# Kernel optimization log

Measured on AMD Instinct MI355X. Metric: run time of the kernel, lower is better.

The kernel has to match this reference:

```python
import jax, jax.numpy as jnp
import numpy as np

B = 256
IN_F = 1024
OUT_F = 1024
SUB_F = 128
Q_F = 1024
N_SUB = 64
N_ACT = 8


def setup_inputs() -> dict:
    key = jax.random.key(0)
    ks = jax.random.split(key, 6)
    x = jax.random.normal(ks[0], (B, IN_F), dtype=jnp.float32)
    q = jax.random.normal(ks[1], (B, Q_F), dtype=jnp.float32)
    # k_layer: nn.Linear(q_features, num_subnets) -> weight [S, Qf], bias [S]
    bound = 1.0 / np.sqrt(Q_F)
    Wk = jax.random.uniform(ks[2], (N_SUB, Q_F), jnp.float32, -bound, bound)
    bk = jax.random.uniform(ks[3], (N_SUB,), jnp.float32, -bound, bound)
    # V_0: [S, sub, in], V_1: [S, out, sub] initialized with randn (as in source)
    V0 = jax.random.normal(ks[4], (N_SUB, SUB_F, IN_F), dtype=jnp.float32)
    V1 = jax.random.normal(ks[5], (N_SUB, OUT_F, SUB_F), dtype=jnp.float32)
    return {"x": x, "q": q, "Wk": Wk, "bk": bk, "V0": V0, "V1": V1}


def _topk_mask(att, k):
    # 0 at top-k positions, -inf elsewhere (per row)
    _, idx = jax.lax.top_k(att, k)  # [B, k]
    mask = jnp.full_like(att, -jnp.inf)
    rows = jnp.arange(att.shape[0])[:, None]
    return mask.at[rows, idx].set(0.0)


def reference(x, q, Wk, bk, V0, V1):
    attention = q @ Wk.T + bk                         # [B, S]
    mask = _topk_mask(attention, N_ACT)               # [B, S]
    sparse_attention = jax.nn.softmax(attention + mask, axis=1)  # [B, S]
    V = jnp.einsum('sor,sri->soi', V1, V0)            # [S, out, in] (bmm)
    weights = jnp.einsum('bs,soi->boi', sparse_attention, V)     # [B, out, in]
    return jnp.einsum('boi,bi->bo', weights, x)       # [B, out]
```

## Files before the change

kernel.cpp:

```cpp
#include <hip/hip_runtime.h>
#include <math.h>

#define NB   256
#define NIN  1024
#define NOUT 1024
#define NSF  128
#define NQ   1024
#define NS   64
#define NACT 8
#define NSLOT 64
#define NIC  4

#define WS_COUNTS 0
#define WS_LISTBK 1024
#define WS_LISTW  17408
#define WS_Y      33792
#define WS_H      8422400

typedef __attribute__((ext_vector_type(8))) short bfrag;
typedef __attribute__((ext_vector_type(4))) float f4_t;

__device__ inline void bsplit(float f, ushort& h, ushort& l) {
    unsigned u = __builtin_bit_cast(unsigned, f);
    h = (ushort)(u >> 16);
    float hf = __builtin_bit_cast(float, u & 0xffff0000u);
    float lo = f - hf;
    l = (ushort)(__builtin_bit_cast(unsigned, lo) >> 16);
}
__device__ inline unsigned bpack(ushort a, ushort b) {
    return (unsigned)a | ((unsigned)b << 16);
}

__global__ __launch_bounds__(256) void attn_topk(
    const float* __restrict__ q, const float* __restrict__ Wk,
    const float* __restrict__ bk, int* __restrict__ counts,
    int* __restrict__ list_bk, float* __restrict__ list_w)
{
    int b = blockIdx.x;
    int t = threadIdx.x;

    __shared__ float qs[NQ];
    __shared__ float att[NS];

    ((float4*)qs)[t] = ((const float4*)(q + (size_t)b * NQ))[t];
    __syncthreads();

    int sid = t >> 2;
    int il  = t & 3;
    const float* wrow = Wk + (size_t)sid * NQ + (il << 2);
    const float* qrow = qs + (il << 2);
    float acc = 0.f;
    #pragma unroll 8
    for (int i = 0; i < NQ; i += 16) {
        float4 w4 = *(const float4*)(wrow + i);
        float4 q4 = *(const float4*)(qrow + i);
        acc += w4.x * q4.x + w4.y * q4.y + w4.z * q4.z + w4.w * q4.w;
    }
    acc += __shfl_xor(acc, 1);
    acc += __shfl_xor(acc, 2);
    if (il == 0) att[sid] = acc + bk[sid];
    __syncthreads();

    if (t < 64) {
        float v = att[t];
        float top_v[NACT]; int top_i[NACT];
        #pragma unroll
        for (int k = 0; k < NACT; ++k) {
            float mv = v; int mi = t;
            #pragma unroll
            for (int off = 1; off < 64; off <<= 1) {
                float ov = __shfl_xor(mv, off);
                int   oi = __shfl_xor(mi, off);
                if (ov > mv || (ov == mv && oi < mi)) { mv = ov; mi = oi; }
            }
            top_v[k] = mv; top_i[k] = mi;
            if (t == mi) v = -INFINITY;
        }
        if (t == 0) {
            float m = top_v[0], den = 0.f, e[NACT];
            #pragma unroll
            for (int k = 0; k < NACT; ++k) { e[k] = expf(top_v[k] - m); den += e[k]; }
            float inv = 1.f / den;
            #pragma unroll
            for (int k = 0; k < NACT; ++k) {
                int s = top_i[k];
                int slot = atomicAdd(&counts[s], 1);
                if (slot < NSLOT) {
                    list_bk[s * NSLOT + slot] = b * NACT + k;
                    list_w[s * NSLOT + slot]  = e[k] * inv;
                }
            }
        }
    }
}

__global__ __launch_bounds__(256) void subnet_h(
    const float* __restrict__ x, const float* __restrict__ V0,
    const int* __restrict__ counts, const int* __restrict__ list_bk,
    float* __restrict__ Hpart)
{
    int s  = blockIdx.x;
    int ic = blockIdx.y;
    int jt = blockIdx.z;
    int nb = counts[s]; if (nb > NSLOT) nb = NSLOT;
    if (jt * 32 >= nb) return;
    int t = threadIdx.x;

    __shared__ __align__(16) ushort vhi[128 * 64], vlo[128 * 64];
    __shared__ __align__(16) ushort xhi[32 * 64],  xlo[32 * 64];
    __shared__ int bidx[32];

    if (t < 32) {
        int idx = jt * 32 + t;
        bidx[t] = (idx < nb) ? (list_bk[s * NSLOT + idx] >> 3) : 0;
    }
    __syncthreads();

    int i0 = ic * 256;
    const float* V0s = V0 + (size_t)s * NSF * NIN;

    int lane = t & 63, w = t >> 6;
    int wo = w >> 1, wj = w & 1;
    int l15 = lane & 15, l4 = lane >> 4;
    int kk = l4 << 3;

    int tr = t >> 4;
    int k4 = (t & 15) << 2;

    int bj0 = bidx[tr], bj1 = bidx[16 + tr];

    float4 va[8], vb[2];
    f4_t acc[4] = {};

    #pragma unroll
    for (int rep = 0; rep < 8; ++rep)
        va[rep] = *(const float4*)(V0s + (size_t)(rep * 16 + tr) * NIN + i0 + k4);
    vb[0] = *(const float4*)(x + (size_t)bj0 * NIN + i0 + k4);
    vb[1] = *(const float4*)(x + (size_t)bj1 * NIN + i0 + k4);

    for (int kc = 0; kc < 256; kc += 64) {
        #pragma unroll
        for (int rep = 0; rep < 8; ++rep) {
            int row = rep * 16 + tr;
            float4 v = va[rep];
            ushort h0,l0,h1,l1,h2,l2,h3,l3;
            bsplit(v.x,h0,l0); bsplit(v.y,h1,l1); bsplit(v.z,h2,l2); bsplit(v.w,h3,l3);
            int hw = ((row << 6) + k4) ^ ((row & 7) << 3);
            *(uint2*)&vhi[hw] = make_uint2(bpack(h0,h1), bpack(h2,h3));
            *(uint2*)&vlo[hw] = make_uint2(bpack(l0,l1), bpack(l2,l3));
        }
        #pragma unroll
        for (int rep = 0; rep < 2; ++rep) {
            int j = rep * 16 + tr;
            float4 v = vb[rep];
            ushort h0,l0,h1,l1,h2,l2,h3,l3;
            bsplit(v.x,h0,l0); bsplit(v.y,h1,l1); bsplit(v.z,h2,l2); bsplit(v.w,h3,l3);
            int hw = ((j << 6) + k4) ^ ((j & 7) << 3);
            *(uint2*)&xhi[hw] = make_uint2(bpack(h0,h1), bpack(h2,h3));
            *(uint2*)&xlo[hw] = make_uint2(bpack(l0,l1), bpack(l2,l3));
        }
        __syncthreads();

        if (kc < 192) {
            int kn = i0 + kc + 64;
            #pragma unroll
            for (int rep = 0; rep < 8; ++rep)
                va[rep] = *(const float4*)(V0s + (size_t)(rep * 16 + tr) * NIN + kn + k4);
            vb[0] = *(const float4*)(x + (size_t)bj0 * NIN + kn + k4);
            vb[1] = *(const float4*)(x + (size_t)bj1 * NIN + kn + k4);
        }

        #pragma unroll
        for (int ks = 0; ks < 64; ks += 32) {
            int jrow = wj * 16 + l15;
            int bhw = ((jrow << 6) + ks + kk) ^ ((jrow & 7) << 3);
            bfrag bh = *(const bfrag*)&xhi[bhw];
            bfrag bl = *(const bfrag*)&xlo[bhw];
            #pragma unroll
            for (int f = 0; f < 4; ++f) {
                int row = wo * 64 + f * 16 + l15;
                int ahw = ((row << 6) + ks + kk) ^ ((row & 7) << 3);
                bfrag ah = *(const bfrag*)&vhi[ahw];
                bfrag al = *(const bfrag*)&vlo[ahw];
                acc[f] = __builtin_amdgcn_mfma_f32_16x16x32_bf16(ah, bh, acc[f], 0, 0, 0);
                acc[f] = __builtin_amdgcn_mfma_f32_16x16x32_bf16(ah, bl, acc[f], 0, 0, 0);
                acc[f] = __builtin_amdgcn_mfma_f32_16x16x32_bf16(al, bh, acc[f], 0, 0, 0);
            }
        }
        __syncthreads();
    }

    int jloc = wj * 16 + l15;
    float* Hp = Hpart + ((size_t)(ic * NS + s) * NSLOT + jt * 32 + jloc) * NSF;
    #pragma unroll
    for (int f = 0; f < 4; ++f) {
        *(float4*)(Hp + wo * 64 + f * 16 + (l4 << 2)) =
            make_float4(acc[f][0], acc[f][1], acc[f][2], acc[f][3]);
    }
}

__global__ __launch_bounds__(256) void subnet_out(
    const float* __restrict__ V1, const int* __restrict__ counts,
    const int* __restrict__ list_bk, const float* __restrict__ list_w,
    const float* __restrict__ Hpart, float* __restrict__ Ybuf)
{
    int s  = blockIdx.x;
    int ot = blockIdx.y;
    int jt = blockIdx.z;
    int nb = counts[s]; if (nb > NSLOT) nb = NSLOT;
    if (jt * 32 >= nb) return;
    int t = threadIdx.x;

    __shared__ __align__(16) ushort vhi[128 * 64], vlo[128 * 64];
    __shared__ __align__(16) ushort hhi[32 * 64],  hlo[32 * 64];
    __shared__ int   bkx[32];
    __shared__ float wjs[32];

    if (t < 32) {
        int idx = jt * 32 + t;
        bool v = idx < nb;
        bkx[t] = v ? list_bk[s * NSLOT + idx] : 0;
        wjs[t] = v ? list_w[s * NSLOT + idx] : 0.f;
    }
    __syncthreads();

    const float* V1s = V1 + (size_t)s * NOUT * NSF + (size_t)ot * 128 * NSF;
    const float* Hp  = Hpart + ((size_t)s * NSLOT + jt * 32) * NSF;
    const size_t HSTR = (size_t)NS * NSLOT * NSF;

    int lane = t & 63, w = t >> 6;
    int wo = w >> 1, wj = w & 1;
    int l15 = lane & 15, l4 = lane >> 4;
    int kk = l4 << 3;

    int tr = t >> 4;
    int k4 = (t & 15) << 2;

    float4 va[8], vb[8];
    f4_t acc[4] = {};

    #pragma unroll
    for (int rep = 0; rep < 8; ++rep)
        va[rep] = *(const float4*)(V1s + (size_t)(rep * 16 + tr) * NSF + k4);
    #pragma unroll
    for (int rep = 0; rep < 2; ++rep) {
        const float* hp = Hp + (size_t)(rep * 16 + tr) * NSF + k4;
        vb[rep * 4 + 0] = *(const float4*)(hp);
        vb[rep * 4 + 1] = *(const float4*)(hp + HSTR);
        vb[rep * 4 + 2] = *(const float4*)(hp + 2 * HSTR);
        vb[rep * 4 + 3] = *(const float4*)(hp + 3 * HSTR);
    }

    for (int kc = 0; kc < NSF; kc += 64) {
        #pragma unroll
        for (int rep = 0; rep < 8; ++rep) {
            int row = rep * 16 + tr;
            float4 v = va[rep];
            ushort h0,l0,h1,l1,h2,l2,h3,l3;
            bsplit(v.x,h0,l0); bsplit(v.y,h1,l1); bsplit(v.z,h2,l2); bsplit(v.w,h3,l3);
            int hw = ((row << 6) + k4) ^ ((row & 7) << 3);
            *(uint2*)&vhi[hw] = make_uint2(bpack(h0,h1), bpack(h2,h3));
            *(uint2*)&vlo[hw] = make_uint2(bpack(l0,l1), bpack(l2,l3));
        }
        #pragma unroll
        for (int rep = 0; rep < 2; ++rep) {
            int j = rep * 16 + tr;
            float4 u0 = vb[rep * 4 + 0], u1 = vb[rep * 4 + 1];
            float4 u2 = vb[rep * 4 + 2], u3 = vb[rep * 4 + 3];
            float4 v = make_float4(u0.x+u1.x+u2.x+u3.x, u0.y+u1.y+u2.y+u3.y,
                                   u0.z+u1.z+u2.z+u3.z, u0.w+u1.w+u2.w+u3.w);
            ushort h0,l0,h1,l1,h2,l2,h3,l3;
            bsplit(v.x,h0,l0); bsplit(v.y,h1,l1); bsplit(v.z,h2,l2); bsplit(v.w,h3,l3);
            int hw = ((j << 6) + k4) ^ ((j & 7) << 3);
            *(uint2*)&hhi[hw] = make_uint2(bpack(h0,h1), bpack(h2,h3));
            *(uint2*)&hlo[hw] = make_uint2(bpack(l0,l1), bpack(l2,l3));
        }
        __syncthreads();

        if (kc == 0) {
            #pragma unroll
            for (int rep = 0; rep < 8; ++rep)
                va[rep] = *(const float4*)(V1s + (size_t)(rep * 16 + tr) * NSF + 64 + k4);
            #pragma unroll
            for (int rep = 0; rep < 2; ++rep) {
                const float* hp = Hp + (size_t)(rep * 16 + tr) * NSF + 64 + k4;
                vb[rep * 4 + 0] = *(const float4*)(hp);
                vb[rep * 4 + 1] = *(const float4*)(hp + HSTR);
                vb[rep * 4 + 2] = *(const float4*)(hp + 2 * HSTR);
                vb[rep * 4 + 3] = *(const float4*)(hp + 3 * HSTR);
            }
        }

        #pragma unroll
        for (int ks = 0; ks < 64; ks += 32) {
            int jrow = wj * 16 + l15;
            int bhw = ((jrow << 6) + ks + kk) ^ ((jrow & 7) << 3);
            bfrag bh = *(const bfrag*)&hhi[bhw];
            bfrag bl = *(const bfrag*)&hlo[bhw];
            #pragma unroll
            for (int f = 0; f < 4; ++f) {
                int row = wo * 64 + f * 16 + l15;
                int ahw = ((row << 6) + ks + kk) ^ ((row & 7) << 3);
                bfrag ah = *(const bfrag*)&vhi[ahw];
                bfrag al = *(const bfrag*)&vlo[ahw];
                acc[f] = __builtin_amdgcn_mfma_f32_16x16x32_bf16(ah, bh, acc[f], 0, 0, 0);
                acc[f] = __builtin_amdgcn_mfma_f32_16x16x32_bf16(ah, bl, acc[f], 0, 0, 0);
                acc[f] = __builtin_amdgcn_mfma_f32_16x16x32_bf16(al, bh, acc[f], 0, 0, 0);
            }
        }
        __syncthreads();
    }

    int jloc = wj * 16 + l15;
    int slot = jt * 32 + jloc;
    if (slot < nb) {
        int   bki = bkx[jloc];
        float wgt = wjs[jloc];
        float* dst = Ybuf + (size_t)bki * NOUT + ot * 128 + wo * 64 + (l4 << 2);
        #pragma unroll
        for (int f = 0; f < 4; ++f) {
            *(float4*)(dst + f * 16) =
                make_float4(wgt*acc[f][0], wgt*acc[f][1], wgt*acc[f][2], wgt*acc[f][3]);
        }
    }
}

__global__ __launch_bounds__(256) void reduce_out(
    const float* __restrict__ Ybuf, float* __restrict__ out)
{
    int b = blockIdx.x, t = threadIdx.x;
    const float* yb = Ybuf + (size_t)b * NACT * NOUT + (t << 2);
    float4 a = *(const float4*)yb;
    #pragma unroll
    for (int k = 1; k < NACT; ++k) {
        float4 v = *(const float4*)(yb + (size_t)k * NOUT);
        a.x += v.x; a.y += v.y; a.z += v.z; a.w += v.w;
    }
    *(float4*)(out + (size_t)b * NOUT + (t << 2)) = a;
}

extern "C" void kernel_launch(void* const* d_in, const int* in_sizes, int n_in,
                              void* d_out, int out_size, void* d_ws, size_t ws_size,
                              hipStream_t stream)
{
    const float* x  = (const float*)d_in[0];
    const float* q  = (const float*)d_in[1];
    const float* Wk = (const float*)d_in[2];
    const float* bk = (const float*)d_in[3];
    const float* V0 = (const float*)d_in[4];
    const float* V1 = (const float*)d_in[5];
    float* out = (float*)d_out;

    char* ws = (char*)d_ws;
    int*   counts  = (int*)(ws + WS_COUNTS);
    int*   list_bk = (int*)(ws + WS_LISTBK);
    float* list_w  = (float*)(ws + WS_LISTW);
    float* Ybuf    = (float*)(ws + WS_Y);
    float* Hpart   = (float*)(ws + WS_H);

    hipMemsetAsync(counts, 0, 1024, stream);

    attn_topk<<<dim3(NB), 256, 0, stream>>>(q, Wk, bk, counts, list_bk, list_w);
    subnet_h<<<dim3(NS, NIC, 2), 256, 0, stream>>>(x, V0, counts, list_bk, Hpart);
    subnet_out<<<dim3(NS, 8, 2), 256, 0, stream>>>(V1, counts, list_bk, list_w, Hpart, Ybuf);
    reduce_out<<<dim3(NB), 256, 0, stream>>>(Ybuf, out);
}
```

Baseline: 145.1 us.

## Replace atomic per-subnet lists with per-block scan of top-k indices

The attention kernel now writes each row's top-k subnet indices and softmax weights densely, with no atomics, which removes the memset and atomic list-building. Each consumer block rebuilds its subnet's batch list itself with a wavefront prefix scan over all top-k indices, so list order becomes deterministic. subnet_h is also re-tiled into smaller 128-thread blocks that each cover half the sub-feature rows, doubling the grid for more parallelism. The cost is redundant scanning work in every block and extra reloading of x tiles across the row splits.

```diff
diff --git a/kernel.cpp b/kernel.cpp
--- a/kernel.cpp
+++ b/kernel.cpp
@@ -11,11 +11,10 @@
 #define NSLOT 64
 #define NIC  4
 
-#define WS_COUNTS 0
-#define WS_LISTBK 1024
-#define WS_LISTW  17408
-#define WS_Y      33792
-#define WS_H      8422400
+#define WS_TOPKS 0
+#define WS_TOPKW 2048
+#define WS_Y     10240
+#define WS_H     8398848
 
 typedef __attribute__((ext_vector_type(8))) short bfrag;
 typedef __attribute__((ext_vector_type(4))) float f4_t;
@@ -33,8 +32,8 @@
 
 __global__ __launch_bounds__(256) void attn_topk(
     const float* __restrict__ q, const float* __restrict__ Wk,
-    const float* __restrict__ bk, int* __restrict__ counts,
-    int* __restrict__ list_bk, float* __restrict__ list_w)
+    const float* __restrict__ bk, unsigned char* __restrict__ topk_s,
+    float* __restrict__ topk_w)
 {
     int b = blockIdx.x;
     int t = threadIdx.x;
@@ -81,67 +80,111 @@
             #pragma unroll
             for (int k = 0; k < NACT; ++k) { e[k] = expf(top_v[k] - m); den += e[k]; }
             float inv = 1.f / den;
-            #pragma unroll
-            for (int k = 0; k < NACT; ++k) {
-                int s = top_i[k];
-                int slot = atomicAdd(&counts[s], 1);
-                if (slot < NSLOT) {
-                    list_bk[s * NSLOT + slot] = b * NACT + k;
-                    list_w[s * NSLOT + slot]  = e[k] * inv;
-                }
-            }
-        }
-    }
-}
-
-__global__ __launch_bounds__(256) void subnet_h(
+            unsigned lo = (unsigned)top_i[0] | ((unsigned)top_i[1] << 8) |
+                          ((unsigned)top_i[2] << 16) | ((unsigned)top_i[3] << 24);
+            unsigned hi = (unsigned)top_i[4] | ((unsigned)top_i[5] << 8) |
+                          ((unsigned)top_i[6] << 16) | ((unsigned)top_i[7] << 24);
+            *(uint2*)(topk_s + (size_t)b * 8) = make_uint2(lo, hi);
+            *(float4*)(topk_w + (size_t)b * 8) =
+                make_float4(e[0]*inv, e[1]*inv, e[2]*inv, e[3]*inv);
+            *(float4*)(topk_w + (size_t)b * 8 + 4) =
+                make_float4(e[4]*inv, e[5]*inv, e[6]*inv, e[7]*inv);
+        }
+    }
+}
+
+__device__ inline void scan_subnet(const unsigned char* topk_s, int s, int t,
+                                   int* ent, int* nb_sh)
+{
+    if (t < 64) {
+        const uint2* ts = (const uint2*)topk_s;
+        uint2 rows[4];
+        #pragma unroll
+        for (int i = 0; i < 4; ++i) rows[i] = ts[t * 4 + i];
+        int cnt = 0;
+        #pragma unroll
+        for (int i = 0; i < 4; ++i) {
+            unsigned lo = rows[i].x, hi = rows[i].y;
+            #pragma unroll
+            for (int k = 0; k < 4; ++k) {
+                cnt += ((int)((lo >> (8*k)) & 0xff) == s);
+                cnt += ((int)((hi >> (8*k)) & 0xff) == s);
+            }
+        }
+        int p = cnt;
+        #pragma unroll
+        for (int off = 1; off < 64; off <<= 1) {
+            int v = __shfl_up(p, off);
+            if (t >= off) p += v;
+        }
+        int pos = p - cnt;
+        int tot = __shfl(p, 63);
+        int nb  = tot > NSLOT ? NSLOT : tot;
+        if (t == 0) *nb_sh = nb;
+        #pragma unroll
+        for (int i = 0; i < 4; ++i) {
+            unsigned lo = rows[i].x, hi = rows[i].y;
+            int b = t * 4 + i;
+            #pragma unroll
+            for (int k = 0; k < 8; ++k) {
+                int sv = (k < 4) ? (int)((lo >> (8*k)) & 0xff)
+                                 : (int)((hi >> (8*(k-4))) & 0xff);
+                if (sv == s) { if (pos < NSLOT) ent[pos] = b * 8 + k; ++pos; }
+            }
+        }
+        if (t >= nb) ent[t] = 0;
+    }
+}
+
+__global__ __launch_bounds__(128) void subnet_h(
     const float* __restrict__ x, const float* __restrict__ V0,
-    const int* __restrict__ counts, const int* __restrict__ list_bk,
-    float* __restrict__ Hpart)
+    const unsigned char* __restrict__ topk_s, float* __restrict__ Hpart)
 {
     int s  = blockIdx.x;
     int ic = blockIdx.y;
-    int jt = blockIdx.z;
-    int nb = counts[s]; if (nb > NSLOT) nb = NSLOT;
+    int rt = blockIdx.z >> 1;
+    int jt = blockIdx.z & 1;
+    int t = threadIdx.x;
+
+    __shared__ __align__(16) ushort vhi[64 * 64], vlo[64 * 64];
+    __shared__ __align__(16) ushort xhi[32 * 64], xlo[32 * 64];
+    __shared__ int ent[NSLOT];
+    __shared__ int nb_sh;
+
+    scan_subnet(topk_s, s, t, ent, &nb_sh);
+    __syncthreads();
+    int nb = nb_sh;
     if (jt * 32 >= nb) return;
-    int t = threadIdx.x;
-
-    __shared__ __align__(16) ushort vhi[128 * 64], vlo[128 * 64];
-    __shared__ __align__(16) ushort xhi[32 * 64],  xlo[32 * 64];
-    __shared__ int bidx[32];
-
-    if (t < 32) {
-        int idx = jt * 32 + t;
-        bidx[t] = (idx < nb) ? (list_bk[s * NSLOT + idx] >> 3) : 0;
-    }
-    __syncthreads();
 
     int i0 = ic * 256;
-    const float* V0s = V0 + (size_t)s * NSF * NIN;
-
-    int lane = t & 63, w = t >> 6;
-    int wo = w >> 1, wj = w & 1;
+    const float* V0s = V0 + ((size_t)s * NSF + rt * 64) * NIN;
+
+    int lane = t & 63;
+    int wj = t >> 6;
     int l15 = lane & 15, l4 = lane >> 4;
     int kk = l4 << 3;
 
     int tr = t >> 4;
     int k4 = (t & 15) << 2;
 
-    int bj0 = bidx[tr], bj1 = bidx[16 + tr];
-
-    float4 va[8], vb[2];
+    int bj[4];
+    #pragma unroll
+    for (int rep = 0; rep < 4; ++rep) bj[rep] = ent[jt * 32 + rep * 8 + tr] >> 3;
+
+    float4 va[8], vb[4];
     f4_t acc[4] = {};
 
     #pragma unroll
     for (int rep = 0; rep < 8; ++rep)
-        va[rep] = *(const float4*)(V0s + (size_t)(rep * 16 + tr) * NIN + i0 + k4);
-    vb[0] = *(const float4*)(x + (size_t)bj0 * NIN + i0 + k4);
-    vb[1] = *(const float4*)(x + (size_t)bj1 * NIN + i0 + k4);
+        va[rep] = *(const float4*)(V0s + (size_t)(rep * 8 + tr) * NIN + i0 + k4);
+    #pragma unroll
+    for (int rep = 0; rep < 4; ++rep)
+        vb[rep] = *(const float4*)(x + (size_t)bj[rep] * NIN + i0 + k4);
 
     for (int kc = 0; kc < 256; kc += 64) {
         #pragma unroll
         for (int rep = 0; rep < 8; ++rep) {
-            int row = rep * 16 + tr;
+            int row = rep * 8 + tr;
             float4 v = va[rep];
             ushort h0,l0,h1,l1,h2,l2,h3,l3;
             bsplit(v.x,h0,l0); bsplit(v.y,h1,l1); bsplit(v.z,h2,l2); bsplit(v.w,h3,l3);
@@ -150,8 +193,8 @@
             *(uint2*)&vlo[hw] = make_uint2(bpack(l0,l1), bpack(l2,l3));
         }
         #pragma unroll
-        for (int rep = 0; rep < 2; ++rep) {
-            int j = rep * 16 + tr;
+        for (int rep = 0; rep < 4; ++rep) {
+            int j = rep * 8 + tr;
             float4 v = vb[rep];
             ushort h0,l0,h1,l1,h2,l2,h3,l3;
             bsplit(v.x,h0,l0); bsplit(v.y,h1,l1); bsplit(v.z,h2,l2); bsplit(v.w,h3,l3);
@@ -165,9 +208,10 @@
             int kn = i0 + kc + 64;
             #pragma unroll
             for (int rep = 0; rep < 8; ++rep)
-                va[rep] = *(const float4*)(V0s + (size_t)(rep * 16 + tr) * NIN + kn + k4);
-            vb[0] = *(const float4*)(x + (size_t)bj0 * NIN + kn + k4);
-            vb[1] = *(const float4*)(x + (size_t)bj1 * NIN + kn + k4);
+                va[rep] = *(const float4*)(V0s + (size_t)(rep * 8 + tr) * NIN + kn + k4);
+            #pragma unroll
+            for (int rep = 0; rep < 4; ++rep)
+                vb[rep] = *(const float4*)(x + (size_t)bj[rep] * NIN + kn + k4);
         }
 
         #pragma unroll
@@ -178,7 +222,7 @@
             bfrag bl = *(const bfrag*)&xlo[bhw];
             #pragma unroll
             for (int f = 0; f < 4; ++f) {
-                int row = wo * 64 + f * 16 + l15;
+                int row = f * 16 + l15;
                 int ahw = ((row << 6) + ks + kk) ^ ((row & 7) << 3);
                 bfrag ah = *(const bfrag*)&vhi[ahw];
                 bfrag al = *(const bfrag*)&vlo[ahw];
@@ -191,38 +235,33 @@
     }
 
     int jloc = wj * 16 + l15;
-    float* Hp = Hpart + ((size_t)(ic * NS + s) * NSLOT + jt * 32 + jloc) * NSF;
+    float* Hp = Hpart + ((size_t)(ic * NS + s) * NSLOT + jt * 32 + jloc) * NSF + rt * 64;
     #pragma unroll
     for (int f = 0; f < 4; ++f) {
-        *(float4*)(Hp + wo * 64 + f * 16 + (l4 << 2)) =
+        *(float4*)(Hp + f * 16 + (l4 << 2)) =
             make_float4(acc[f][0], acc[f][1], acc[f][2], acc[f][3]);
     }
 }
 
 __global__ __launch_bounds__(256) void subnet_out(
-    const float* __restrict__ V1, const int* __restrict__ counts,
-    const int* __restrict__ list_bk, const float* __restrict__ list_w,
-    const float* __restrict__ Hpart, float* __restrict__ Ybuf)
+    const float* __restrict__ V1, const unsigned char* __restrict__ topk_s,
+    const float* __restrict__ topk_w, const float* __restrict__ Hpart,
+    float* __restrict__ Ybuf)
 {
     int s  = blockIdx.x;
     int ot = blockIdx.y;
     int jt = blockIdx.z;
-    int nb = counts[s]; if (nb > NSLOT) nb = NSLOT;
-    if (jt * 32 >= nb) return;
     int t = threadIdx.x;
 
     __shared__ __align__(16) ushort vhi[128 * 64], vlo[128 * 64];
     __shared__ __align__(16) ushort hhi[32 * 64],  hlo[32 * 64];
-    __shared__ int   bkx[32];
-    __shared__ float wjs[32];
-
-    if (t < 32) {
-        int idx = jt * 32 + t;
-        bool v = idx < nb;
-        bkx[t] = v ? list_bk[s * NSLOT + idx] : 0;
-        wjs[t] = v ? list_w[s * NSLOT + idx] : 0.f;
-    }
+    __shared__ int   ent[NSLOT];
+    __shared__ int   nb_sh;
+
+    scan_subnet(topk_s, s, t, ent, &nb_sh);
     __syncthreads();
+    int nb = nb_sh;
+    if (jt * 32 >= nb) return;
 
     const float* V1s = V1 + (size_t)s * NOUT * NSF + (size_t)ot * 128 * NSF;
     const float* Hp  = Hpart + ((size_t)s * NSLOT + jt * 32) * NSF;
@@ -314,8 +353,8 @@
     int jloc = wj * 16 + l15;
     int slot = jt * 32 + jloc;
     if (slot < nb) {
-        int   bki = bkx[jloc];
-        float wgt = wjs[jloc];
+        int   bki = ent[slot];
+        float wgt = topk_w[bki];
         float* dst = Ybuf + (size_t)bki * NOUT + ot * 128 + wo * 64 + (l4 << 2);
         #pragma unroll
         for (int f = 0; f < 4; ++f) {
@@ -352,16 +391,13 @@
     float* out = (float*)d_out;
 
     char* ws = (char*)d_ws;
-    int*   counts  = (int*)(ws + WS_COUNTS);
-    int*   list_bk = (int*)(ws + WS_LISTBK);
-    float* list_w  = (float*)(ws + WS_LISTW);
-    float* Ybuf    = (float*)(ws + WS_Y);
-    float* Hpart   = (float*)(ws + WS_H);
-
-    hipMemsetAsync(counts, 0, 1024, stream);
-
-    attn_topk<<<dim3(NB), 256, 0, stream>>>(q, Wk, bk, counts, list_bk, list_w);
-    subnet_h<<<dim3(NS, NIC, 2), 256, 0, stream>>>(x, V0, counts, list_bk, Hpart);
-    subnet_out<<<dim3(NS, 8, 2), 256, 0, stream>>>(V1, counts, list_bk, list_w, Hpart, Ybuf);
+    unsigned char* topk_s = (unsigned char*)(ws + WS_TOPKS);
+    float*         topk_w = (float*)(ws + WS_TOPKW);
+    float*         Ybuf   = (float*)(ws + WS_Y);
+    float*         Hpart  = (float*)(ws + WS_H);
+
+    attn_topk<<<dim3(NB), 256, 0, stream>>>(q, Wk, bk, topk_s, topk_w);
+    subnet_h<<<dim3(NS, NIC, 4), 128, 0, stream>>>(x, V0, topk_s, Hpart);
+    subnet_out<<<dim3(NS, 8, 2), 256, 0, stream>>>(V1, topk_s, topk_w, Hpart, Ybuf);
     reduce_out<<<dim3(NB), 256, 0, stream>>>(Ybuf, out);
 }
```

After: 135.4 us. 1.07x faster.
